# Performance work log

Measured on AMD Instinct MI355X. Metric: run time of the kernel, lower is better.

Reference implementation:

```python
import jax, jax.numpy as jnp
import numpy as np
from jax import lax

NB = 8          # num_blocks
THRESH = 0.01   # sparsity_threshold


def _clinear(z, wr, wi, bias):
    # complex linear y = z @ W^T + b with W = wr + i*wi, z complex
    # (c+id)(a+ib) = (ca - db) + i(cb + da)  -- same math as the torch
    # Karatsuba decomposition (k1-k3, k1+k2).
    zr, zi = z.real, z.imag
    yr = jnp.einsum('...i,oi->...o', zr, wr) - jnp.einsum('...i,oi->...o', zi, wi)
    yi = jnp.einsum('...i,oi->...o', zr, wi) + jnp.einsum('...i,oi->...o', zi, wr)
    y = lax.complex(yr, yi)
    return y + lax.complex(bias[:, 0], bias[:, 1])


def _softshrink(v, t):
    return jnp.where(v > t, v - t, jnp.where(v < -t, v + t, jnp.zeros_like(v)))


def setup_inputs() -> dict:
    key = jax.random.key(0)
    ks = jax.random.split(key, 7)
    B, H, W, D = 4, 128, 128, 768
    bs = D // NB          # block_size = 96
    hid = bs              # hidden_size_factor = 1.0
    scale = np.sqrt(0.5).astype(np.float32)
    kaiming = 1.0 / np.sqrt(bs)
    x = jax.random.normal(ks[0], (B, H, W, D), dtype=jnp.float32)
    # ComplexLinear weights: nn.Linear init then scaled by sqrt(0.5)
    w1r = jax.random.uniform(ks[1], (hid, bs), jnp.float32, -kaiming, kaiming) * scale
    w1i = jax.random.uniform(ks[2], (hid, bs), jnp.float32, -kaiming, kaiming) * scale
    b1 = jax.random.normal(ks[3], (hid, 2), dtype=jnp.float32) * 0.02
    kaiming2 = 1.0 / np.sqrt(hid)
    w2r = jax.random.uniform(ks[4], (bs, hid), jnp.float32, -kaiming2, kaiming2) * scale
    w2i = jax.random.uniform(ks[5], (bs, hid), jnp.float32, -kaiming2, kaiming2) * scale
    b2 = jax.random.normal(ks[6], (bs, 2), dtype=jnp.float32) * 0.02
    return {"x": x, "w1r": w1r, "w1i": w1i, "b1": b1,
            "w2r": w2r, "w2i": w2i, "b2": b2}


def reference(x, w1r, w1i, b1, w2r, w2i, b2):
    B, H, W, D = x.shape
    bs = D // NB
    bias = x  # direct_skip=True -> identity skip
    # ortho-normalized real FFT over spatial dims (1,2)
    xf = jnp.fft.rfftn(x, s=(H, W), axes=(1, 2), norm='ortho')  # [B,H,Fw,D] c64
    Fw = xf.shape[2]
    xb = xf.reshape(B, H, Fw, NB, bs)
    h = _clinear(xb, w1r, w1i, b1)
    h = lax.complex(jax.nn.relu(h.real), jax.nn.relu(h.imag))  # ComplexReLU
    y = _clinear(h, w2r, w2i, b2)
    y = y.reshape(B, H, Fw, D)
    # componentwise softshrink (by_magnitude=False)
    y = lax.complex(_softshrink(y.real, THRESH), _softshrink(y.imag, THRESH))
    out = jnp.fft.irfftn(y, s=(H, W), axes=(1, 2), norm='ortho')
    return out + bias
```

## Files before the change

kernel.cpp:

```cpp
#include <hip/hip_runtime.h>
#include <hip/hip_bf16.h>
#include <cstdio>

#define TPB 256
#define B_ 4
#define H_ 128
#define W_ 128
#define D_ 768
#define FW 65
#define BH_ 512
#define THRESH_ 0.01f
#define NEG_TWO_PI_OVER_128 (-0.04908738521234052f)

typedef short bf16x8 __attribute__((ext_vector_type(8)));
typedef float f32x4 __attribute__((ext_vector_type(4)));


__device__ __forceinline__ unsigned pk(float lo, float hi) {
  __hip_bfloat162 h2 = __float22bfloat162_rn(make_float2(lo, hi));
  return *(unsigned*)&h2;
}
__device__ __forceinline__ float2 upk(unsigned u) {
  return __bfloat1622float2(*(__hip_bfloat162*)&u);
}
__device__ __forceinline__ int drev(int k) {
  return ((k & 3) << 5) | (((k >> 2) & 3) << 3) | (((k >> 4) & 3) << 1) | ((k >> 6) & 1);
}
__device__ __forceinline__ int drevinv(int s) {
  return ((s & 1) << 6) | (((s >> 1) & 3) << 4) | (((s >> 3) & 3) << 2) | ((s >> 5) & 3);
}

template <bool FWD>
__device__ __forceinline__ void bf4reg(float& x0r, float& x0i, float& x1r, float& x1i,
                                       float& x2r, float& x2i, float& x3r, float& x3i,
                                       float c1, float s1, float c2, float s2, float c3, float s3) {
  const float v0r = x0r + x2r, v0i = x0i + x2i, v2r = x0r - x2r, v2i = x0i - x2i;
  const float v1r = x1r + x3r, v1i = x1i + x3i, v3r = x1r - x3r, v3i = x1i - x3i;
  float u1r, u1i, u3r, u3i;
  if (FWD) { u1r = v2r + v3i; u1i = v2i - v3r; u3r = v2r - v3i; u3i = v2i + v3r; }
  else     { u1r = v2r - v3i; u1i = v2i + v3r; u3r = v2r + v3i; u3i = v2i - v3r; }
  const float u2r = v0r - v1r, u2i = v0i - v1i;
  x0r = v0r + v1r;            x0i = v0i + v1i;
  x1r = u1r * c1 - u1i * s1;  x1i = u1r * s1 + u1i * c1;
  x2r = u2r * c2 - u2i * s2;  x2i = u2r * s2 + u2i * c2;
  x3r = u3r * c3 - u3i * s3;  x3i = u3r * s3 + u3i * c3;
}

__device__ __forceinline__ void ibf4r(float& x0r, float& x0i, float& x1r, float& x1i,
                                      float& x2r, float& x2i, float& x3r, float& x3i,
                                      float c1, float s1, float c2, float s2, float c3, float s3) {
  const float t0r = x0r, t0i = x0i;
  const float t1r = x1r * c1 + x1i * s1, t1i = x1i * c1 - x1r * s1;
  const float t2r = x2r * c2 + x2i * s2, t2i = x2i * c2 - x2r * s2;
  const float t3r = x3r * c3 + x3i * s3, t3i = x3i * c3 - x3r * s3;
  const float w0r = t0r + t2r, w0i = t0i + t2i, w2r = t0r - t2r, w2i = t0i - t2i;
  const float w1r = t1r + t3r, w1i = t1i + t3i, w3r = t1r - t3r, w3i = t1i - t3i;
  x0r = w0r + w1r; x0i = w0i + w1i;
  x1r = w2r - w3i; x1i = w2i + w3r;
  x2r = w0r - w1r; x2i = w0i - w1i;
  x3r = w2r + w3i; x3i = w2i - w3r;
}

#define TW_INIT() do { if (t < 128) { float s_, c_; \
    __sincosf(NEG_TWO_PI_OVER_128 * (float)t, &s_, &c_); twr[t] = c_; twi[t] = s_; } } while (0)

__global__ __launch_bounds__(TPB) void k_wpack(const float* __restrict__ w1r,
                                               const float* __restrict__ w1i,
                                               const float* __restrict__ w2r,
                                               const float* __restrict__ w2i,
                                               unsigned short* __restrict__ wp) {
  const int tid = blockIdx.x * TPB + threadIdx.x;
  if (tid >= 2 * 36864) return;
  const int L = tid / 36864, rem = tid % 36864;
  const int n = rem / 192, k = rem % 192;
  const int c = k >> 1, s = k & 1, o = n >> 1, t = n & 1;
  const float* wr = L ? w2r : w1r;
  const float* wi = L ? w2i : w1i;
  const float val = (s == 0) ? (t == 0 ? wr[o * 96 + c] : wi[o * 96 + c])
                             : (t == 0 ? -wi[o * 96 + c] : wr[o * 96 + c]);
  __hip_bfloat16 h = __float2bfloat16(val);
  const int idx = ((n * 6 + (k >> 5)) * 4 + ((k >> 3) & 3)) * 8 + (k & 7);
  wp[L * 36864 + idx] = *(unsigned short*)&h;
}

__global__ __launch_bounds__(TPB) void k_fwd_w(const float* __restrict__ x,
                                               unsigned* __restrict__ fq) {
  __shared__ float re[4096], im[4096], twr[128], twi[128];
  const int t = threadIdx.x;
  const int bh = blockIdx.x;
  const int d0 = blockIdx.y << 6;
  TW_INIT();
  const int c = t & 31, p = t >> 5;
  const float2* xp = (const float2*)(x + (size_t)bh * 98304 + d0);

  float vr[4][4], vi[4][4];
#pragma unroll
  for (int q = 0; q < 4; ++q)
#pragma unroll
    for (int m = 0; m < 4; ++m) {
      const float2 v = xp[(p + 8 * m + 32 * q) * 384 + c];
      vr[q][m] = v.x; vi[q][m] = v.y;
    }
  __syncthreads();
#pragma unroll
  for (int m = 0; m < 4; ++m) {
    const int np = p + 8 * m;
    bf4reg<true>(vr[0][m], vi[0][m], vr[1][m], vi[1][m], vr[2][m], vi[2][m], vr[3][m], vi[3][m],
                 twr[np], twi[np], twr[2 * np], twi[2 * np], twr[3 * np], twi[3 * np]);
  }
#pragma unroll
  for (int q = 0; q < 4; ++q)
    bf4reg<true>(vr[q][0], vi[q][0], vr[q][1], vi[q][1], vr[q][2], vi[q][2], vr[q][3], vi[q][3],
                 twr[4 * p], twi[4 * p], twr[8 * p], twi[8 * p], twr[12 * p], twi[12 * p]);
#pragma unroll
  for (int q = 0; q < 4; ++q)
#pragma unroll
    for (int m = 0; m < 4; ++m) {
      const int pos = p + 8 * m + 32 * q;
      re[pos * 32 + c] = vr[q][m]; im[pos * 32 + c] = vi[q][m];
    }
  __syncthreads();

#pragma unroll
  for (int half = 0; half < 2; ++half) {
    const int g = 8 * half + p;
    float wr8[8], wi8[8];
#pragma unroll
    for (int j = 0; j < 8; ++j) { wr8[j] = re[(8 * g + j) * 32 + c]; wi8[j] = im[(8 * g + j) * 32 + c]; }
    bf4reg<true>(wr8[0], wi8[0], wr8[2], wi8[2], wr8[4], wi8[4], wr8[6], wi8[6],
                 1.f, 0.f, 1.f, 0.f, 1.f, 0.f);
    bf4reg<true>(wr8[1], wi8[1], wr8[3], wi8[3], wr8[5], wi8[5], wr8[7], wi8[7],
                 twr[16], twi[16], twr[32], twi[32], twr[48], twi[48]);
#pragma unroll
    for (int j = 0; j < 8; j += 2) {
      const float ar = wr8[j], ai = wi8[j], br = wr8[j + 1], bi = wi8[j + 1];
      wr8[j] = ar + br; wi8[j] = ai + bi;
      wr8[j + 1] = ar - br; wi8[j + 1] = ai - bi;
    }
#pragma unroll
    for (int j = 0; j < 8; ++j) {
      re[(8 * g + j) * 32 + c] = wr8[j]; im[(8 * g + j) * 32 + c] = wi8[j];
    }
  }
  __syncthreads();

#pragma unroll
  for (int it = 0; it < 9; ++it) {
    const int idx = it * TPB + t;
    if (idx < FW * 32) {
      const int q = idx >> 5, cc = idx & 31;
      const int sq = drev(q), smm = drev((128 - q) & 127);
      const float a = re[sq * 32 + cc], b = im[sq * 32 + cc];
      const float cr = re[smm * 32 + cc], dr = -im[smm * 32 + cc];
      const float hsc = 0.00390625f;
      const float xer = (a + cr) * hsc, xei = (b + dr) * hsc;
      const float xor_ = (b - dr) * hsc, xoi = (cr - a) * hsc;
      *(uint2*)(fq + (size_t)(bh * FW + q) * 768 + d0 + 2 * cc) =
          make_uint2(pk(xer, xei), pk(xor_, xoi));
    }
  }
}

__global__ __launch_bounds__(TPB) void k_fwd_h(unsigned* __restrict__ fq) {
  __shared__ float re[4096], im[4096], twr[128], twi[128];
  const int t = threadIdx.x;
  const int b = blockIdx.x, fw = blockIdx.y, d0 = blockIdx.z << 5;
  TW_INIT();
  unsigned* fp = fq + (size_t)(b * 128 * FW + fw) * 768 + d0;
  const int c = t & 31, p = t >> 5;
  const size_t hs = (size_t)FW * 768;

  float vr[4][4], vi[4][4];
#pragma unroll
  for (int q = 0; q < 4; ++q)
#pragma unroll
    for (int m = 0; m < 4; ++m) {
      const float2 v = upk(fp[(size_t)(p + 8 * m + 32 * q) * hs + c]);
      vr[q][m] = v.x; vi[q][m] = v.y;
    }
  __syncthreads();
#pragma unroll
  for (int m = 0; m < 4; ++m) {
    const int np = p + 8 * m;
    bf4reg<true>(vr[0][m], vi[0][m], vr[1][m], vi[1][m], vr[2][m], vi[2][m], vr[3][m], vi[3][m],
                 twr[np], twi[np], twr[2 * np], twi[2 * np], twr[3 * np], twi[3 * np]);
  }
#pragma unroll
  for (int q = 0; q < 4; ++q)
    bf4reg<true>(vr[q][0], vi[q][0], vr[q][1], vi[q][1], vr[q][2], vi[q][2], vr[q][3], vi[q][3],
                 twr[4 * p], twi[4 * p], twr[8 * p], twi[8 * p], twr[12 * p], twi[12 * p]);
#pragma unroll
  for (int q = 0; q < 4; ++q)
#pragma unroll
    for (int m = 0; m < 4; ++m) {
      const int pos = p + 8 * m + 32 * q;
      re[pos * 32 + c] = vr[q][m]; im[pos * 32 + c] = vi[q][m];
    }
  __syncthreads();

#pragma unroll
  for (int half = 0; half < 2; ++half) {
    const int g = 8 * half + p;
    float wr8[8], wi8[8];
#pragma unroll
    for (int j = 0; j < 8; ++j) { wr8[j] = re[(8 * g + j) * 32 + c]; wi8[j] = im[(8 * g + j) * 32 + c]; }
    bf4reg<true>(wr8[0], wi8[0], wr8[2], wi8[2], wr8[4], wi8[4], wr8[6], wi8[6],
                 1.f, 0.f, 1.f, 0.f, 1.f, 0.f);
    bf4reg<true>(wr8[1], wi8[1], wr8[3], wi8[3], wr8[5], wi8[5], wr8[7], wi8[7],
                 twr[16], twi[16], twr[32], twi[32], twr[48], twi[48]);
#pragma unroll
    for (int j = 0; j < 8; j += 2) {
      const float ar = wr8[j], ai = wi8[j], br = wr8[j + 1], bi = wi8[j + 1];
      wr8[j] = ar + br; wi8[j] = ai + bi;
      wr8[j + 1] = ar - br; wi8[j + 1] = ai - bi;
    }
#pragma unroll
    for (int j = 0; j < 8; ++j)
      fp[(size_t)(8 * g + j) * hs + c] = pk(wr8[j], wi8[j]);
  }
}

__global__ __launch_bounds__(TPB, 4) void k_mlp_mfma(unsigned* __restrict__ fq,
    const bf16x8* __restrict__ wpb,
    const float* __restrict__ b1, const float* __restrict__ b2) {
  __shared__ __align__(16) char lds[24576];
  const int t  = threadIdx.x;
  const int wv = t >> 6;
  const int l  = t & 63;
  const int c16 = l & 15, g = l >> 4, low3 = l & 7;
  const int n0 = wv * 48;
  const int P0 = blockIdx.x << 6;

  const uint4* src = (const uint4*)(fq + (size_t)P0 * 96);
#pragma unroll
  for (int it = 0; it < 6; ++it) {
    const int q = it * TPB + t;
    const int row = q / 24, f = q % 24;
    *(uint4*)(lds + row * 384 + ((f * 16) ^ ((row & 7) << 4))) = src[q];
  }
  __syncthreads();

  f32x4 acc[4][3];
  float bs0 = b1[n0 + c16], bs1 = b1[n0 + 16 + c16], bs2 = b1[n0 + 32 + c16];

#pragma unroll
  for (int mt = 0; mt < 4; ++mt)
#pragma unroll
    for (int np = 0; np < 3; ++np) acc[mt][np] = (f32x4)0.f;
  for (int kk = 0; kk < 6; ++kk) {
    bf16x8 a[4];
#pragma unroll
    for (int mt = 0; mt < 4; ++mt) {
      const int row = (mt << 4) + c16;
      a[mt] = *(const bf16x8*)(lds + row * 384 + ((kk * 64 + g * 16) ^ (low3 << 4)));
    }
    bf16x8 bfr[3];
#pragma unroll
    for (int np = 0; np < 3; ++np) bfr[np] = wpb[((n0 + np * 16 + c16) * 6 + kk) * 4 + g];
#pragma unroll
    for (int mt = 0; mt < 4; ++mt)
#pragma unroll
      for (int np = 0; np < 3; ++np)
        acc[mt][np] = __builtin_amdgcn_mfma_f32_16x16x32_bf16(a[mt], bfr[np], acc[mt][np], 0, 0, 0);
  }
  __syncthreads();
#pragma unroll
  for (int mt = 0; mt < 4; ++mt)
#pragma unroll
    for (int np = 0; np < 3; ++np) {
      const int col = n0 + np * 16 + c16;
      const float bb = np == 0 ? bs0 : (np == 1 ? bs1 : bs2);
#pragma unroll
      for (int r = 0; r < 4; ++r) {
        const int row = (mt << 4) + (g << 2) + r;
        const float vv = fmaxf(acc[mt][np][r] + bb, 0.f);
        __hip_bfloat16 hb = __float2bfloat16(vv);
        *(unsigned short*)(lds + row * 384 + ((2 * col) ^ ((row & 7) << 4))) = *(unsigned short*)&hb;
      }
    }
  __syncthreads();

  bs0 = b2[n0 + c16]; bs1 = b2[n0 + 16 + c16]; bs2 = b2[n0 + 32 + c16];
#pragma unroll
  for (int mt = 0; mt < 4; ++mt)
#pragma unroll
    for (int np = 0; np < 3; ++np) acc[mt][np] = (f32x4)0.f;
  const bf16x8* wpb2 = wpb + 4608;
  for (int kk = 0; kk < 6; ++kk) {
    bf16x8 a[4];
#pragma unroll
    for (int mt = 0; mt < 4; ++mt) {
      const int row = (mt << 4) + c16;
      a[mt] = *(const bf16x8*)(lds + row * 384 + ((kk * 64 + g * 16) ^ (low3 << 4)));
    }
    bf16x8 bfr[3];
#pragma unroll
    for (int np = 0; np < 3; ++np) bfr[np] = wpb2[((n0 + np * 16 + c16) * 6 + kk) * 4 + g];
#pragma unroll
    for (int mt = 0; mt < 4; ++mt)
#pragma unroll
      for (int np = 0; np < 3; ++np)
        acc[mt][np] = __builtin_amdgcn_mfma_f32_16x16x32_bf16(a[mt], bfr[np], acc[mt][np], 0, 0, 0);
  }
  unsigned short* fq16 = (unsigned short*)fq;
#pragma unroll
  for (int mt = 0; mt < 4; ++mt)
#pragma unroll
    for (int np = 0; np < 3; ++np) {
      const int col = n0 + np * 16 + c16;
      const float bb = np == 0 ? bs0 : (np == 1 ? bs1 : bs2);
#pragma unroll
      for (int r = 0; r < 4; ++r) {
        const int row = (mt << 4) + (g << 2) + r;
        float vv = acc[mt][np][r] + bb;
        vv = (vv > THRESH_) ? (vv - THRESH_) : ((vv < -THRESH_) ? (vv + THRESH_) : 0.f);
        __hip_bfloat16 hb = __float2bfloat16(vv);
        fq16[(size_t)(P0 + row) * 192 + col] = *(unsigned short*)&hb;
      }
    }
}

__global__ __launch_bounds__(TPB) void k_inv_h(unsigned* __restrict__ fq) {
  __shared__ float re[4096], im[4096], twr[128], twi[128];
  const int t = threadIdx.x;
  const int b = blockIdx.x, fw = blockIdx.y, d0 = blockIdx.z << 5;
  TW_INIT();
  unsigned* fp = fq + (size_t)(b * 128 * FW + fw) * 768 + d0;
  const int c = t & 31, p = t >> 5;
  const size_t hs = (size_t)FW * 768;

#pragma unroll
  for (int half = 0; half < 2; ++half) {
    const int g = 8 * half + p;
    float wr8[8], wi8[8];
#pragma unroll
    for (int j = 0; j < 8; ++j) {
      const float2 v = upk(fp[(size_t)(8 * g + j) * hs + c]);
      wr8[j] = v.x; wi8[j] = v.y;
    }
    if (half == 0) __syncthreads();
#pragma unroll
    for (int j = 0; j < 8; j += 2) {
      const float ar = wr8[j], ai = wi8[j], br = wr8[j + 1], bi = wi8[j + 1];
      wr8[j] = ar + br; wi8[j] = ai + bi;
      wr8[j + 1] = ar - br; wi8[j + 1] = ai - bi;
    }
    ibf4r(wr8[0], wi8[0], wr8[2], wi8[2], wr8[4], wi8[4], wr8[6], wi8[6],
          1.f, 0.f, 1.f, 0.f, 1.f, 0.f);
    ibf4r(wr8[1], wi8[1], wr8[3], wi8[3], wr8[5], wi8[5], wr8[7], wi8[7],
          twr[16], twi[16], twr[32], twi[32], twr[48], twi[48]);
#pragma unroll
    for (int j = 0; j < 8; ++j) {
      re[(8 * g + j) * 32 + c] = wr8[j]; im[(8 * g + j) * 32 + c] = wi8[j];
    }
  }
  __syncthreads();

  float vr[4][4], vi[4][4];
#pragma unroll
  for (int q = 0; q < 4; ++q)
#pragma unroll
    for (int m = 0; m < 4; ++m) {
      const int pos = p + 8 * m + 32 * q;
      vr[q][m] = re[pos * 32 + c]; vi[q][m] = im[pos * 32 + c];
    }
#pragma unroll
  for (int q = 0; q < 4; ++q)
    ibf4r(vr[q][0], vi[q][0], vr[q][1], vi[q][1], vr[q][2], vi[q][2], vr[q][3], vi[q][3],
          twr[4 * p], twi[4 * p], twr[8 * p], twi[8 * p], twr[12 * p], twi[12 * p]);
#pragma unroll
  for (int m = 0; m < 4; ++m) {
    const int np = p + 8 * m;
    ibf4r(vr[0][m], vi[0][m], vr[1][m], vi[1][m], vr[2][m], vi[2][m], vr[3][m], vi[3][m],
          twr[np], twi[np], twr[2 * np], twi[2 * np], twr[3 * np], twi[3 * np]);
  }
#pragma unroll
  for (int q = 0; q < 4; ++q)
#pragma unroll
    for (int m = 0; m < 4; ++m)
      fp[(size_t)(p + 8 * m + 32 * q) * hs + c] = pk(vr[q][m], vi[q][m]);
}

__global__ __launch_bounds__(TPB) void k_inv_w(const unsigned* __restrict__ fq,
                                               const float* __restrict__ x,
                                               float* __restrict__ out) {
  __shared__ float re[4096], im[4096], twr[128], twi[128];
  const int t = threadIdx.x;
  const int bh = blockIdx.x;
  const int d0 = blockIdx.y << 6;
  TW_INIT();
  const int c = t & 31, p = t >> 5;
  const float sc = 0.0078125f;

#pragma unroll
  for (int it = 0; it < 9; ++it) {
    const int idx = it * TPB + t;
    if (idx < FW * 32) {
      const int q = idx >> 5, cc = idx & 31;
      const uint2 vv = *(const uint2*)(fq + (size_t)(bh * FW + q) * 768 + d0 + 2 * cc);
      const float2 e = upk(vv.x), o = upk(vv.y);
      re[q * 32 + cc] = (e.x - o.y) * sc; im[q * 32 + cc] = (e.y + o.x) * sc;
      if (q >= 1 && q <= 63) {
        re[(128 - q) * 32 + cc] = (e.x + o.y) * sc;
        im[(128 - q) * 32 + cc] = (o.x - e.y) * sc;
      }
    }
  }
  __syncthreads();

  float vr[4][4], vi[4][4];
#pragma unroll
  for (int q = 0; q < 4; ++q)
#pragma unroll
    for (int m = 0; m < 4; ++m) {
      const int pos = p + 8 * m + 32 * q;
      vr[q][m] = re[pos * 32 + c]; vi[q][m] = im[pos * 32 + c];
    }
#pragma unroll
  for (int m = 0; m < 4; ++m) {
    const int np = p + 8 * m;
    bf4reg<false>(vr[0][m], vi[0][m], vr[1][m], vi[1][m], vr[2][m], vi[2][m], vr[3][m], vi[3][m],
                  twr[np], -twi[np], twr[2 * np], -twi[2 * np], twr[3 * np], -twi[3 * np]);
  }
#pragma unroll
  for (int q = 0; q < 4; ++q)
    bf4reg<false>(vr[q][0], vi[q][0], vr[q][1], vi[q][1], vr[q][2], vi[q][2], vr[q][3], vi[q][3],
                  twr[4 * p], -twi[4 * p], twr[8 * p], -twi[8 * p], twr[12 * p], -twi[12 * p]);
#pragma unroll
  for (int q = 0; q < 4; ++q)
#pragma unroll
    for (int m = 0; m < 4; ++m) {
      const int pos = p + 8 * m + 32 * q;
      re[pos * 32 + c] = vr[q][m]; im[pos * 32 + c] = vi[q][m];
    }
  __syncthreads();

  const float2* xv = (const float2*)x;
  float2* ov = (float2*)out;
#pragma unroll
  for (int half = 0; half < 2; ++half) {
    const int g = 8 * half + p;
    float wr8[8], wi8[8];
#pragma unroll
    for (int j = 0; j < 8; ++j) { wr8[j] = re[(8 * g + j) * 32 + c]; wi8[j] = im[(8 * g + j) * 32 + c]; }
    bf4reg<false>(wr8[0], wi8[0], wr8[2], wi8[2], wr8[4], wi8[4], wr8[6], wi8[6],
                  1.f, 0.f, 1.f, 0.f, 1.f, 0.f);
    bf4reg<false>(wr8[1], wi8[1], wr8[3], wi8[3], wr8[5], wi8[5], wr8[7], wi8[7],
                  twr[16], -twi[16], twr[32], -twi[32], twr[48], -twi[48]);
#pragma unroll
    for (int j = 0; j < 8; j += 2) {
      const float ar = wr8[j], ai = wi8[j], br = wr8[j + 1], bi = wi8[j + 1];
      wr8[j] = ar + br; wi8[j] = ai + bi;
      wr8[j + 1] = ar - br; wi8[j + 1] = ai - bi;
    }
#pragma unroll
    for (int j = 0; j < 8; ++j) {
      const int w = drevinv(8 * g + j);
      const size_t fi = (size_t)bh * 49152 + w * 384 + (d0 >> 1) + c;
      const float2 s = xv[fi];
      ov[fi] = make_float2(wr8[j] + s.x, wi8[j] + s.y);
    }
  }
}

extern "C" void kernel_launch(void* const* d_in, const int* in_sizes, int n_in,
                              void* d_out, int out_size, void* d_ws, size_t ws_size,
                              hipStream_t stream) {
  const float* x   = (const float*)d_in[0];
  const float* w1r = (const float*)d_in[1];
  const float* w1i = (const float*)d_in[2];
  const float* b1  = (const float*)d_in[3];
  const float* w2r = (const float*)d_in[4];
  const float* w2i = (const float*)d_in[5];
  const float* b2  = (const float*)d_in[6];
  unsigned* fq = (unsigned*)d_ws;
  float* out = (float*)d_out;

  const size_t need = (size_t)BH_ * FW * 768 * 4;
  if (ws_size < need) {
    fprintf(stderr, "kernel_launch: ws too small (%zu < %zu)\n", ws_size, need);
    return;
  }

  unsigned short* wp = (unsigned short*)d_out;

  k_wpack<<<dim3(288), TPB, 0, stream>>>(w1r, w1i, w2r, w2i, wp);
  k_fwd_w<<<dim3(BH_, 12), TPB, 0, stream>>>(x, fq);
  k_fwd_h<<<dim3(B_, FW, 24), TPB, 0, stream>>>(fq);
  k_mlp_mfma<<<dim3(4160), TPB, 0, stream>>>(fq, (const bf16x8*)wp, b1, b2);
  k_inv_h<<<dim3(B_, FW, 24), TPB, 0, stream>>>(fq);
  k_inv_w<<<dim3(BH_, 12), TPB, 0, stream>>>(fq, x, out);
}
```

Baseline: 323.9 us.

## Fuse H-axis FFT, complex MLP, and inverse H-axis FFT into one kernel

Measured after the change: 408.8 us. 1.26x slower.

```diff
diff --git a/kernel.cpp b/kernel.cpp
--- a/kernel.cpp
+++ b/kernel.cpp
@@ -161,224 +161,248 @@
   }
 }
 
-__global__ __launch_bounds__(TPB) void k_fwd_h(unsigned* __restrict__ fq) {
-  __shared__ float re[4096], im[4096], twr[128], twi[128];
-  const int t = threadIdx.x;
-  const int b = blockIdx.x, fw = blockIdx.y, d0 = blockIdx.z << 5;
-  TW_INIT();
-  unsigned* fp = fq + (size_t)(b * 128 * FW + fw) * 768 + d0;
-  const int c = t & 31, p = t >> 5;
-  const size_t hs = (size_t)FW * 768;
-
-  float vr[4][4], vi[4][4];
-#pragma unroll
-  for (int q = 0; q < 4; ++q)
-#pragma unroll
-    for (int m = 0; m < 4; ++m) {
-      const float2 v = upk(fp[(size_t)(p + 8 * m + 32 * q) * hs + c]);
-      vr[q][m] = v.x; vi[q][m] = v.y;
-    }
-  __syncthreads();
-#pragma unroll
-  for (int m = 0; m < 4; ++m) {
-    const int np = p + 8 * m;
-    bf4reg<true>(vr[0][m], vi[0][m], vr[1][m], vi[1][m], vr[2][m], vi[2][m], vr[3][m], vi[3][m],
-                 twr[np], twi[np], twr[2 * np], twi[2 * np], twr[3 * np], twi[3 * np]);
-  }
-#pragma unroll
-  for (int q = 0; q < 4; ++q)
-    bf4reg<true>(vr[q][0], vi[q][0], vr[q][1], vi[q][1], vr[q][2], vi[q][2], vr[q][3], vi[q][3],
-                 twr[4 * p], twi[4 * p], twr[8 * p], twi[8 * p], twr[12 * p], twi[12 * p]);
-#pragma unroll
-  for (int q = 0; q < 4; ++q)
-#pragma unroll
-    for (int m = 0; m < 4; ++m) {
-      const int pos = p + 8 * m + 32 * q;
-      re[pos * 32 + c] = vr[q][m]; im[pos * 32 + c] = vi[q][m];
-    }
-  __syncthreads();
-
-#pragma unroll
-  for (int half = 0; half < 2; ++half) {
-    const int g = 8 * half + p;
-    float wr8[8], wi8[8];
-#pragma unroll
-    for (int j = 0; j < 8; ++j) { wr8[j] = re[(8 * g + j) * 32 + c]; wi8[j] = im[(8 * g + j) * 32 + c]; }
-    bf4reg<true>(wr8[0], wi8[0], wr8[2], wi8[2], wr8[4], wi8[4], wr8[6], wi8[6],
-                 1.f, 0.f, 1.f, 0.f, 1.f, 0.f);
-    bf4reg<true>(wr8[1], wi8[1], wr8[3], wi8[3], wr8[5], wi8[5], wr8[7], wi8[7],
-                 twr[16], twi[16], twr[32], twi[32], twr[48], twi[48]);
-#pragma unroll
-    for (int j = 0; j < 8; j += 2) {
-      const float ar = wr8[j], ai = wi8[j], br = wr8[j + 1], bi = wi8[j + 1];
-      wr8[j] = ar + br; wi8[j] = ai + bi;
-      wr8[j + 1] = ar - br; wi8[j + 1] = ai - bi;
-    }
-#pragma unroll
-    for (int j = 0; j < 8; ++j)
-      fp[(size_t)(8 * g + j) * hs + c] = pk(wr8[j], wi8[j]);
-  }
-}
-
-__global__ __launch_bounds__(TPB, 4) void k_mlp_mfma(unsigned* __restrict__ fq,
+__global__ __launch_bounds__(384) void k_mid2(unsigned* __restrict__ fq,
     const bf16x8* __restrict__ wpb,
     const float* __restrict__ b1, const float* __restrict__ b2) {
-  __shared__ __align__(16) char lds[24576];
-  const int t  = threadIdx.x;
-  const int wv = t >> 6;
-  const int l  = t & 63;
-  const int c16 = l & 15, g = l >> 4, low3 = l & 7;
-  const int n0 = wv * 48;
-  const int P0 = blockIdx.x << 6;
-
-  const uint4* src = (const uint4*)(fq + (size_t)P0 * 96);
-#pragma unroll
-  for (int it = 0; it < 6; ++it) {
-    const int q = it * TPB + t;
-    const int row = q / 24, f = q % 24;
-    *(uint4*)(lds + row * 384 + ((f * 16) ^ ((row & 7) << 4))) = src[q];
-  }
-  __syncthreads();
-
-  f32x4 acc[4][3];
-  float bs0 = b1[n0 + c16], bs1 = b1[n0 + 16 + c16], bs2 = b1[n0 + 32 + c16];
-
-#pragma unroll
-  for (int mt = 0; mt < 4; ++mt)
-#pragma unroll
-    for (int np = 0; np < 3; ++np) acc[mt][np] = (f32x4)0.f;
+  __shared__ __align__(16) char abuf[49152];
+  __shared__ float twr[128], twi[128];
+  const int t = threadIdx.x;
+  const int blk = blockIdx.x, fw = blockIdx.y, b = blockIdx.z;
+  TW_INIT();
+  const int cG = t >> 6, pp = (t >> 4) & 3, cL = t & 15;
+  const int c = cG * 16 + cL;
+  unsigned* fp = fq + ((size_t)(b * 128) * FW + fw) * 768 + blk * 96;
+  const size_t hs = (size_t)FW * 768;
+
+  const float rS2 = 0.70710678118654752f;
+  const int bp = pp & 1;
+  const bool lo = (pp < 2);
+  const float cA = lo ? 1.f : (bp ? rS2 : 1.f);
+  const float sA = lo ? 0.f : (bp ? -rS2 : 0.f);
+  const float cB = lo ? (bp ? 0.f : 1.f) : (bp ? -rS2 : 1.f);
+  const float sB = lo ? (bp ? -1.f : 0.f) : (bp ? -rS2 : 0.f);
+
+  float vr[2][4][4], vi[2][4][4];
+
+#pragma unroll
+  for (int j0 = 0; j0 < 2; ++j0)
+#pragma unroll
+    for (int q = 0; q < 4; ++q)
+#pragma unroll
+      for (int m = 0; m < 4; ++m) {
+        const int pos = pp + 4 * j0 + 8 * m + 32 * q;
+        const float2 v = upk(fp[(size_t)pos * hs + c]);
+        vr[j0][q][m] = v.x; vi[j0][q][m] = v.y;
+      }
+  __syncthreads();
+
+#pragma unroll
+  for (int j0 = 0; j0 < 2; ++j0)
+#pragma unroll
+    for (int m = 0; m < 4; ++m) {
+      const int np = pp + 4 * j0 + 8 * m;
+      bf4reg<true>(vr[j0][0][m], vi[j0][0][m], vr[j0][1][m], vi[j0][1][m],
+                   vr[j0][2][m], vi[j0][2][m], vr[j0][3][m], vi[j0][3][m],
+                   twr[np], twi[np], twr[2 * np], twi[2 * np], twr[3 * np], twi[3 * np]);
+    }
+#pragma unroll
+  for (int j0 = 0; j0 < 2; ++j0) {
+    const int np8 = pp + 4 * j0;
+#pragma unroll
+    for (int q = 0; q < 4; ++q)
+      bf4reg<true>(vr[j0][q][0], vi[j0][q][0], vr[j0][q][1], vi[j0][q][1],
+                   vr[j0][q][2], vi[j0][q][2], vr[j0][q][3], vi[j0][q][3],
+                   twr[4 * np8], twi[4 * np8], twr[8 * np8], twi[8 * np8],
+                   twr[12 * np8], twi[12 * np8]);
+  }
+#pragma unroll
+  for (int q = 0; q < 4; ++q)
+#pragma unroll
+    for (int m = 0; m < 4; ++m) {
+      const float sr = vr[0][q][m] + vr[1][q][m], si = vi[0][q][m] + vi[1][q][m];
+      const float dr = vr[0][q][m] - vr[1][q][m], di = vi[0][q][m] - vi[1][q][m];
+      const float txr = lo ? dr : sr, txi = lo ? di : si;
+      const float rxr = __shfl_xor(txr, 32), rxi = __shfl_xor(txi, 32);
+      if (lo) {
+        vr[0][q][m] = sr + rxr; vi[0][q][m] = si + rxi;
+        const float ur = sr - rxr, ui = si - rxi;
+        vr[1][q][m] = ur * cB - ui * sB; vi[1][q][m] = ur * sB + ui * cB;
+      } else {
+        const float u1r = rxr + di, u1i = rxi - dr;
+        const float u3r = rxr - di, u3i = rxi + dr;
+        vr[0][q][m] = u1r * cA - u1i * sA; vi[0][q][m] = u1r * sA + u1i * cA;
+        vr[1][q][m] = u3r * cB - u3i * sB; vi[1][q][m] = u3r * sB + u3i * cB;
+      }
+    }
+#pragma unroll
+  for (int j0 = 0; j0 < 2; ++j0)
+#pragma unroll
+    for (int q = 0; q < 4; ++q)
+#pragma unroll
+      for (int m = 0; m < 4; ++m) {
+        const float rr = __shfl_xor(vr[j0][q][m], 16);
+        const float ri = __shfl_xor(vi[j0][q][m], 16);
+        vr[j0][q][m] = bp ? (rr - vr[j0][q][m]) : (vr[j0][q][m] + rr);
+        vi[j0][q][m] = bp ? (ri - vi[j0][q][m]) : (vi[j0][q][m] + ri);
+      }
+#pragma unroll
+  for (int j0 = 0; j0 < 2; ++j0)
+#pragma unroll
+    for (int q = 0; q < 4; ++q)
+#pragma unroll
+      for (int m = 0; m < 4; ++m) {
+        const int row = pp + 4 * j0 + 8 * m + 32 * q;
+        *(unsigned*)(abuf + row * 384 + ((4 * c) ^ ((row & 7) << 4))) =
+            pk(vr[j0][q][m], vi[j0][q][m]);
+      }
+  __syncthreads();
+
+  const int wv = t >> 6, l = t & 63;
+  const int c16 = l & 15, g = l >> 4;
+  const int n0 = wv * 32;
+  f32x4 acc[8][2];
+  float bs0 = b1[n0 + c16], bs1 = b1[n0 + 16 + c16];
+
+#pragma unroll
+  for (int mt = 0; mt < 8; ++mt) { acc[mt][0] = (f32x4)0.f; acc[mt][1] = (f32x4)0.f; }
   for (int kk = 0; kk < 6; ++kk) {
-    bf16x8 a[4];
-#pragma unroll
-    for (int mt = 0; mt < 4; ++mt) {
+    bf16x8 a[8];
+#pragma unroll
+    for (int mt = 0; mt < 8; ++mt) {
       const int row = (mt << 4) + c16;
-      a[mt] = *(const bf16x8*)(lds + row * 384 + ((kk * 64 + g * 16) ^ (low3 << 4)));
-    }
-    bf16x8 bfr[3];
-#pragma unroll
-    for (int np = 0; np < 3; ++np) bfr[np] = wpb[((n0 + np * 16 + c16) * 6 + kk) * 4 + g];
-#pragma unroll
-    for (int mt = 0; mt < 4; ++mt)
-#pragma unroll
-      for (int np = 0; np < 3; ++np)
-        acc[mt][np] = __builtin_amdgcn_mfma_f32_16x16x32_bf16(a[mt], bfr[np], acc[mt][np], 0, 0, 0);
-  }
-  __syncthreads();
-#pragma unroll
-  for (int mt = 0; mt < 4; ++mt)
-#pragma unroll
-    for (int np = 0; np < 3; ++np) {
+      a[mt] = *(const bf16x8*)(abuf + row * 384 + ((kk * 64 + g * 16) ^ ((row & 7) << 4)));
+    }
+    const bf16x8 bf0 = wpb[((n0 + c16) * 6 + kk) * 4 + g];
+    const bf16x8 bf1 = wpb[((n0 + 16 + c16) * 6 + kk) * 4 + g];
+#pragma unroll
+    for (int mt = 0; mt < 8; ++mt) {
+      acc[mt][0] = __builtin_amdgcn_mfma_f32_16x16x32_bf16(a[mt], bf0, acc[mt][0], 0, 0, 0);
+      acc[mt][1] = __builtin_amdgcn_mfma_f32_16x16x32_bf16(a[mt], bf1, acc[mt][1], 0, 0, 0);
+    }
+  }
+  __syncthreads();
+#pragma unroll
+  for (int mt = 0; mt < 8; ++mt)
+#pragma unroll
+    for (int np = 0; np < 2; ++np) {
       const int col = n0 + np * 16 + c16;
-      const float bb = np == 0 ? bs0 : (np == 1 ? bs1 : bs2);
+      const float bb = np ? bs1 : bs0;
 #pragma unroll
       for (int r = 0; r < 4; ++r) {
         const int row = (mt << 4) + (g << 2) + r;
         const float vv = fmaxf(acc[mt][np][r] + bb, 0.f);
         __hip_bfloat16 hb = __float2bfloat16(vv);
-        *(unsigned short*)(lds + row * 384 + ((2 * col) ^ ((row & 7) << 4))) = *(unsigned short*)&hb;
-      }
-    }
-  __syncthreads();
-
-  bs0 = b2[n0 + c16]; bs1 = b2[n0 + 16 + c16]; bs2 = b2[n0 + 32 + c16];
-#pragma unroll
-  for (int mt = 0; mt < 4; ++mt)
-#pragma unroll
-    for (int np = 0; np < 3; ++np) acc[mt][np] = (f32x4)0.f;
+        *(unsigned short*)(abuf + row * 384 + ((2 * col) ^ ((row & 7) << 4))) = *(unsigned short*)&hb;
+      }
+    }
+  __syncthreads();
+
+  bs0 = b2[n0 + c16]; bs1 = b2[n0 + 16 + c16];
+#pragma unroll
+  for (int mt = 0; mt < 8; ++mt) { acc[mt][0] = (f32x4)0.f; acc[mt][1] = (f32x4)0.f; }
   const bf16x8* wpb2 = wpb + 4608;
   for (int kk = 0; kk < 6; ++kk) {
-    bf16x8 a[4];
-#pragma unroll
-    for (int mt = 0; mt < 4; ++mt) {
+    bf16x8 a[8];
+#pragma unroll
+    for (int mt = 0; mt < 8; ++mt) {
       const int row = (mt << 4) + c16;
-      a[mt] = *(const bf16x8*)(lds + row * 384 + ((kk * 64 + g * 16) ^ (low3 << 4)));
-    }
-    bf16x8 bfr[3];
-#pragma unroll
-    for (int np = 0; np < 3; ++np) bfr[np] = wpb2[((n0 + np * 16 + c16) * 6 + kk) * 4 + g];
-#pragma unroll
-    for (int mt = 0; mt < 4; ++mt)
-#pragma unroll
-      for (int np = 0; np < 3; ++np)
-        acc[mt][np] = __builtin_amdgcn_mfma_f32_16x16x32_bf16(a[mt], bfr[np], acc[mt][np], 0, 0, 0);
-  }
-  unsigned short* fq16 = (unsigned short*)fq;
-#pragma unroll
-  for (int mt = 0; mt < 4; ++mt)
-#pragma unroll
-    for (int np = 0; np < 3; ++np) {
+      a[mt] = *(const bf16x8*)(abuf + row * 384 + ((kk * 64 + g * 16) ^ ((row & 7) << 4)));
+    }
+    const bf16x8 bf0 = wpb2[((n0 + c16) * 6 + kk) * 4 + g];
+    const bf16x8 bf1 = wpb2[((n0 + 16 + c16) * 6 + kk) * 4 + g];
+#pragma unroll
+    for (int mt = 0; mt < 8; ++mt) {
+      acc[mt][0] = __builtin_amdgcn_mfma_f32_16x16x32_bf16(a[mt], bf0, acc[mt][0], 0, 0, 0);
+      acc[mt][1] = __builtin_amdgcn_mfma_f32_16x16x32_bf16(a[mt], bf1, acc[mt][1], 0, 0, 0);
+    }
+  }
+  __syncthreads();
+#pragma unroll
+  for (int mt = 0; mt < 8; ++mt)
+#pragma unroll
+    for (int np = 0; np < 2; ++np) {
       const int col = n0 + np * 16 + c16;
-      const float bb = np == 0 ? bs0 : (np == 1 ? bs1 : bs2);
+      const float bb = np ? bs1 : bs0;
 #pragma unroll
       for (int r = 0; r < 4; ++r) {
         const int row = (mt << 4) + (g << 2) + r;
         float vv = acc[mt][np][r] + bb;
         vv = (vv > THRESH_) ? (vv - THRESH_) : ((vv < -THRESH_) ? (vv + THRESH_) : 0.f);
         __hip_bfloat16 hb = __float2bfloat16(vv);
-        fq16[(size_t)(P0 + row) * 192 + col] = *(unsigned short*)&hb;
-      }
-    }
-}
-
-__global__ __launch_bounds__(TPB) void k_inv_h(unsigned* __restrict__ fq) {
-  __shared__ float re[4096], im[4096], twr[128], twi[128];
-  const int t = threadIdx.x;
-  const int b = blockIdx.x, fw = blockIdx.y, d0 = blockIdx.z << 5;
-  TW_INIT();
-  unsigned* fp = fq + (size_t)(b * 128 * FW + fw) * 768 + d0;
-  const int c = t & 31, p = t >> 5;
-  const size_t hs = (size_t)FW * 768;
-
-#pragma unroll
-  for (int half = 0; half < 2; ++half) {
-    const int g = 8 * half + p;
-    float wr8[8], wi8[8];
-#pragma unroll
-    for (int j = 0; j < 8; ++j) {
-      const float2 v = upk(fp[(size_t)(8 * g + j) * hs + c]);
-      wr8[j] = v.x; wi8[j] = v.y;
-    }
-    if (half == 0) __syncthreads();
-#pragma unroll
-    for (int j = 0; j < 8; j += 2) {
-      const float ar = wr8[j], ai = wi8[j], br = wr8[j + 1], bi = wi8[j + 1];
-      wr8[j] = ar + br; wi8[j] = ai + bi;
-      wr8[j + 1] = ar - br; wi8[j + 1] = ai - bi;
-    }
-    ibf4r(wr8[0], wi8[0], wr8[2], wi8[2], wr8[4], wi8[4], wr8[6], wi8[6],
-          1.f, 0.f, 1.f, 0.f, 1.f, 0.f);
-    ibf4r(wr8[1], wi8[1], wr8[3], wi8[3], wr8[5], wi8[5], wr8[7], wi8[7],
-          twr[16], twi[16], twr[32], twi[32], twr[48], twi[48]);
-#pragma unroll
-    for (int j = 0; j < 8; ++j) {
-      re[(8 * g + j) * 32 + c] = wr8[j]; im[(8 * g + j) * 32 + c] = wi8[j];
-    }
-  }
-  __syncthreads();
-
-  float vr[4][4], vi[4][4];
-#pragma unroll
-  for (int q = 0; q < 4; ++q)
-#pragma unroll
-    for (int m = 0; m < 4; ++m) {
-      const int pos = p + 8 * m + 32 * q;
-      vr[q][m] = re[pos * 32 + c]; vi[q][m] = im[pos * 32 + c];
-    }
-#pragma unroll
-  for (int q = 0; q < 4; ++q)
-    ibf4r(vr[q][0], vi[q][0], vr[q][1], vi[q][1], vr[q][2], vi[q][2], vr[q][3], vi[q][3],
-          twr[4 * p], twi[4 * p], twr[8 * p], twi[8 * p], twr[12 * p], twi[12 * p]);
-#pragma unroll
-  for (int m = 0; m < 4; ++m) {
-    const int np = p + 8 * m;
-    ibf4r(vr[0][m], vi[0][m], vr[1][m], vi[1][m], vr[2][m], vi[2][m], vr[3][m], vi[3][m],
-          twr[np], twi[np], twr[2 * np], twi[2 * np], twr[3 * np], twi[3 * np]);
-  }
-#pragma unroll
-  for (int q = 0; q < 4; ++q)
-#pragma unroll
-    for (int m = 0; m < 4; ++m)
-      fp[(size_t)(p + 8 * m + 32 * q) * hs + c] = pk(vr[q][m], vi[q][m]);
+        *(unsigned short*)(abuf + row * 384 + ((2 * col) ^ ((row & 7) << 4))) = *(unsigned short*)&hb;
+      }
+    }
+  __syncthreads();
+
+#pragma unroll
+  for (int j0 = 0; j0 < 2; ++j0)
+#pragma unroll
+    for (int q = 0; q < 4; ++q)
+#pragma unroll
+      for (int m = 0; m < 4; ++m) {
+        const int row = pp + 4 * j0 + 8 * m + 32 * q;
+        const float2 v = upk(*(unsigned*)(abuf + row * 384 + ((4 * c) ^ ((row & 7) << 4))));
+        vr[j0][q][m] = v.x; vi[j0][q][m] = v.y;
+      }
+#pragma unroll
+  for (int j0 = 0; j0 < 2; ++j0)
+#pragma unroll
+    for (int q = 0; q < 4; ++q)
+#pragma unroll
+      for (int m = 0; m < 4; ++m) {
+        const float rr = __shfl_xor(vr[j0][q][m], 16);
+        const float ri = __shfl_xor(vi[j0][q][m], 16);
+        vr[j0][q][m] = bp ? (rr - vr[j0][q][m]) : (vr[j0][q][m] + rr);
+        vi[j0][q][m] = bp ? (ri - vi[j0][q][m]) : (vi[j0][q][m] + ri);
+      }
+#pragma unroll
+  for (int q = 0; q < 4; ++q)
+#pragma unroll
+    for (int m = 0; m < 4; ++m) {
+      const float a0r = vr[0][q][m] * cA + vi[0][q][m] * sA;
+      const float a0i = vi[0][q][m] * cA - vr[0][q][m] * sA;
+      const float a1r = vr[1][q][m] * cB + vi[1][q][m] * sB;
+      const float a1i = vi[1][q][m] * cB - vr[1][q][m] * sB;
+      const float wsr = a0r + a1r, wsi = a0i + a1i;
+      const float wdr = a0r - a1r, wdi = a0i - a1i;
+      const float txr = lo ? wdr : wsr, txi = lo ? wdi : wsi;
+      const float rxr = __shfl_xor(txr, 32), rxi = __shfl_xor(txi, 32);
+      if (lo) {
+        vr[0][q][m] = wsr + rxr; vi[0][q][m] = wsi + rxi;
+        vr[1][q][m] = wsr - rxr; vi[1][q][m] = wsi - rxi;
+      } else {
+        vr[0][q][m] = rxr - wdi; vi[0][q][m] = rxi + wdr;
+        vr[1][q][m] = rxr + wdi; vi[1][q][m] = rxi - wdr;
+      }
+    }
+#pragma unroll
+  for (int j0 = 0; j0 < 2; ++j0) {
+    const int np8 = pp + 4 * j0;
+#pragma unroll
+    for (int q = 0; q < 4; ++q)
+      ibf4r(vr[j0][q][0], vi[j0][q][0], vr[j0][q][1], vi[j0][q][1],
+            vr[j0][q][2], vi[j0][q][2], vr[j0][q][3], vi[j0][q][3],
+            twr[4 * np8], twi[4 * np8], twr[8 * np8], twi[8 * np8],
+            twr[12 * np8], twi[12 * np8]);
+  }
+#pragma unroll
+  for (int j0 = 0; j0 < 2; ++j0)
+#pragma unroll
+    for (int m = 0; m < 4; ++m) {
+      const int np = pp + 4 * j0 + 8 * m;
+      ibf4r(vr[j0][0][m], vi[j0][0][m], vr[j0][1][m], vi[j0][1][m],
+            vr[j0][2][m], vi[j0][2][m], vr[j0][3][m], vi[j0][3][m],
+            twr[np], twi[np], twr[2 * np], twi[2 * np], twr[3 * np], twi[3 * np]);
+    }
+#pragma unroll
+  for (int j0 = 0; j0 < 2; ++j0)
+#pragma unroll
+    for (int q = 0; q < 4; ++q)
+#pragma unroll
+      for (int m = 0; m < 4; ++m) {
+        const int pos = pp + 4 * j0 + 8 * m + 32 * q;
+        fp[(size_t)pos * hs + c] = pk(vr[j0][q][m], vi[j0][q][m]);
+      }
 }
 
 __global__ __launch_bounds__(TPB) void k_inv_w(const unsigned* __restrict__ fq,
@@ -486,8 +510,6 @@
 
   k_wpack<<<dim3(288), TPB, 0, stream>>>(w1r, w1i, w2r, w2i, wp);
   k_fwd_w<<<dim3(BH_, 12), TPB, 0, stream>>>(x, fq);
-  k_fwd_h<<<dim3(B_, FW, 24), TPB, 0, stream>>>(fq);
-  k_mlp_mfma<<<dim3(4160), TPB, 0, stream>>>(fq, (const bf16x8*)wp, b1, b2);
-  k_inv_h<<<dim3(B_, FW, 24), TPB, 0, stream>>>(fq);
+  k_mid2<<<dim3(8, FW, B_), 384, 0, stream>>>(fq, (const bf16x8*)wp, b1, b2);
   k_inv_w<<<dim3(BH_, 12), TPB, 0, stream>>>(fq, x, out);
 }
```
